# Optimization experiments

Measured on AMD Instinct MI355X. Metric: run time of the kernel, lower is better.

## Reference

```python
import jax, jax.numpy as jnp
import numpy as np

N_NODES = 100000


def _gcn_norm(edges, n_nodes):
    # PyG GCNConv: add self-loops, symmetric normalization D^{-1/2}(A+I)D^{-1/2}
    loop = jnp.arange(n_nodes, dtype=edges.dtype)
    src = jnp.concatenate([edges[0], loop])
    dst = jnp.concatenate([edges[1], loop])
    ones = jnp.ones(src.shape[0], dtype=jnp.float32)
    deg = jax.ops.segment_sum(ones, dst, num_segments=n_nodes)  # >=1 thanks to self-loops
    dinv = jax.lax.rsqrt(deg)
    norm = dinv[src] * dinv[dst]  # [E + N]
    return src, dst, norm


def _gcn_conv(x, W, b, src, dst, norm, n_nodes):
    # lin -> gather -> scale -> scatter-add -> +bias (PyG GCNConv order)
    h = x @ W                                   # [N, D_out]
    msg = h[src] * norm[:, None]                # [E+N, D_out]
    agg = jax.ops.segment_sum(msg, dst, num_segments=n_nodes)
    return agg + b


def setup_inputs() -> dict:
    key = jax.random.key(0)
    k_x, k_e, k_w1, k_w2 = jax.random.split(key, 4)
    F_in, D_hid, n_labels, n_edges = 128, 128, 32, 625000
    features = jax.random.normal(k_x, (N_NODES, F_in), dtype=jnp.float32)
    edges = jax.random.randint(k_e, (2, n_edges), 0, N_NODES, dtype=jnp.int64)
    W1 = jax.random.normal(k_w1, (F_in, D_hid), dtype=jnp.float32) / np.sqrt(F_in)
    b1 = jnp.zeros((D_hid,), dtype=jnp.float32)
    W2 = jax.random.normal(k_w2, (D_hid, n_labels), dtype=jnp.float32) / np.sqrt(D_hid)
    b2 = jnp.zeros((n_labels,), dtype=jnp.float32)
    return {"features": features, "edges": edges, "W1": W1, "b1": b1, "W2": W2, "b2": b2}


def reference(features, edges, W1, b1, W2, b2):
    n_nodes = features.shape[0]
    src, dst, norm = _gcn_norm(edges, n_nodes)
    h1 = jax.nn.relu(_gcn_conv(features, W1, b1, src, dst, norm, n_nodes))
    h2 = _gcn_conv(h1, W2, b2, src, dst, norm, n_nodes)
    return jax.nn.log_softmax(h2, axis=1)
```

## Files before the change

### kernel.cpp

```cpp
#include <hip/hip_runtime.h>

#define NN 100000
#define MAXDEG 32

typedef _Float16 f16;
typedef f16 f16x2 __attribute__((ext_vector_type(2)));
typedef f16 f16x8 __attribute__((ext_vector_type(8)));
typedef float f32x4 __attribute__((ext_vector_type(4)));

__device__ __forceinline__ int detect_is64(const void* edges, int E) {
    const long long* p = (const long long*)edges;
    int m = E < 1024 ? E : 1024;
    int bad = 0;
    for (int i = (threadIdx.x & 63); i < m; i += 64) {
        if ((unsigned long long)p[i] >= (unsigned long long)NN) bad = 1;
    }
    return !__any(bad);
}

__device__ __forceinline__ int edge_at(const void* e, long i, int is64) {
    return is64 ? (int)((const long long*)e)[i] : ((const int*)e)[i];
}

__global__ __launch_bounds__(256) void k_prep(const float* __restrict__ W1,
                                              const float* __restrict__ W2,
                                              f16* __restrict__ BT1,
                                              f16* __restrict__ BT2,
                                              int* __restrict__ deg, int n) {
    int t = blockIdx.x * blockDim.x + threadIdx.x;
    int stride = gridDim.x * blockDim.x;
    for (int i = t; i < n; i += stride) deg[i] = 0;
    for (int i = t; i < 128 * 128; i += stride) {
        int nn = i >> 7, kk = i & 127;
        BT1[i] = (f16)W1[kk * 128 + nn];
    }
    for (int i = t; i < 32 * 128; i += stride) {
        int nn = i >> 7, kk = i & 127;
        BT2[i] = (f16)W2[kk * 32 + nn];
    }
}

__global__ __launch_bounds__(256) void k_dg1(const float* __restrict__ X,
                                             const f16* __restrict__ BT,
                                             f16* __restrict__ H, int n,
                                             const void* edges, int E,
                                             int* __restrict__ deg,
                                             int* __restrict__ slot,
                                             int nG, int nD) {
    __shared__ __align__(16) unsigned char Bs[16384];
    const int bid = blockIdx.x;
    const int lo = nG < nD ? nG : nD;
    int gid = -1, fid = -1;
    if (bid < 2 * lo) {
        if ((bid & 1) == 0) gid = bid >> 1; else fid = bid >> 1;
    } else if (nG > nD) {
        gid = bid - lo;
    } else {
        fid = bid - lo;
    }

    if (fid >= 0) {
        int is64 = detect_is64(edges, E);
        long stride = (long)nD * 256;
        for (long e = (long)fid * 256 + threadIdx.x; e < E; e += stride) {
            int d = edge_at(edges, (long)E + e, is64);
            int t = atomicAdd(&deg[d], 1);
            slot[e] = (t < MAXDEG) ? d * MAXDEG + t : -1;
        }
        return;
    }

    const int tid = threadIdx.x;
    const int wave = tid >> 6;
    const int lane = tid & 63;
    const int lrow = lane & 15;
    const int kgrp = lane >> 4;
    const int row0 = gid * 64 + wave * 16;
    int arow = row0 + lrow;
    if (arow >= n) arow = n - 1;

    f16x8 a[4];
#pragma unroll
    for (int ks = 0; ks < 4; ks++) {
        const float* ap = &X[(long)arow * 128 + ks * 32 + kgrp * 8];
        float4 v0 = *(const float4*)ap;
        float4 v1 = *(const float4*)(ap + 4);
        f16x8 tv;
        tv[0] = (f16)v0.x; tv[1] = (f16)v0.y; tv[2] = (f16)v0.z; tv[3] = (f16)v0.w;
        tv[4] = (f16)v1.x; tv[5] = (f16)v1.y; tv[6] = (f16)v1.z; tv[7] = (f16)v1.w;
        a[ks] = tv;
    }

    const int sw = (lrow & 7) << 4;
#pragma unroll
    for (int half = 0; half < 2; half++) {
#pragma unroll
        for (int s = 0; s < 4; s++) {
            int L = (tid + s * 256) * 16;
            int row = L >> 8;
            f16x8 v = *(const f16x8*)((const unsigned char*)BT + half * 16384 + L);
            *(f16x8*)(Bs + (L ^ ((row & 7) << 4))) = v;
        }
        __syncthreads();
#pragma unroll
        for (int ntl = 0; ntl < 4; ntl++) {
            f32x4 acc = {0.f, 0.f, 0.f, 0.f};
            const int bbase = (ntl * 16 + lrow) * 256 + kgrp * 16;
#pragma unroll
            for (int ks = 0; ks < 4; ks++) {
                f16x8 b = *(const f16x8*)(Bs + ((bbase + ks * 64) ^ sw));
                acc = __builtin_amdgcn_mfma_f32_16x16x32_f16(a[ks], b, acc, 0, 0, 0);
            }
            const int col = (half * 4 + ntl) * 16 + lrow;
#pragma unroll
            for (int r = 0; r < 4; r++) {
                int grow = row0 + kgrp * 4 + r;
                if (grow < n) H[(long)grow * 128 + col] = (f16)acc[r];
            }
        }
        __syncthreads();
    }
}

__global__ void k_fill(const void* edges, int E,
                       const int* __restrict__ slot,
                       int* __restrict__ csr) {
    int is64 = detect_is64(edges, E);
    for (long e = blockIdx.x * (long)blockDim.x + threadIdx.x; e < E;
         e += (long)gridDim.x * blockDim.x) {
        int s = edge_at(edges, e, is64);
        int sl = slot[e];
        if (sl >= 0) csr[sl] = s;
    }
}

__global__ __launch_bounds__(256) void k_sg(const f16* __restrict__ H,
                                            const int* __restrict__ deg,
                                            const int* __restrict__ csr,
                                            const float* __restrict__ b1,
                                            const f16* __restrict__ BT2,
                                            f16* __restrict__ H2, int n) {
    __shared__ __align__(16) unsigned char As[16384];
    __shared__ __align__(16) unsigned char Bs[8192];
    const int tid = threadIdx.x;
    {
        int L = tid * 16;
        int row = L >> 8;
        *(f16x8*)(Bs + (L ^ ((row & 7) << 4))) =
            *(const f16x8*)((const unsigned char*)BT2 + L);
        L += 4096; row = L >> 8;
        *(f16x8*)(Bs + (L ^ ((row & 7) << 4))) =
            *(const f16x8*)((const unsigned char*)BT2 + L);
    }

    const int tile0 = blockIdx.x * 64;
    const int lane16 = tid & 15;
    const int ngrp = tid >> 4;
    const f16x8* H8 = (const f16x8*)H;
    const float4 bl = *(const float4*)&b1[lane16 * 8];
    const float4 bh = *(const float4*)&b1[lane16 * 8 + 4];

#pragma unroll
    for (int sub = 0; sub < 4; sub++) {
        const int lrowA = sub * 16 + ngrp;
        int node = tile0 + lrowA;
        int nd = node < n ? node : n - 1;
        int dg = deg[nd];
        float di = rsqrtf((float)(dg + 1));
        float w0 = di * di;
        f16x8 self = H8[(long)nd * 16 + lane16];
        float acc0[8], acc1[8], acc2[8], acc3[8];
#pragma unroll
        for (int j = 0; j < 8; j++) {
            acc0[j] = w0 * (float)self[j];
            acc1[j] = 0.f; acc2[j] = 0.f; acc3[j] = 0.f;
        }
        int s0 = nd * MAXDEG;
        int cnt = dg < MAXDEG ? dg : MAXDEG;
        int s1 = s0 + cnt;
        for (int i = s0; i < s1; i += 4) {
            int i1 = i + 1 < s1 ? i + 1 : s1 - 1;
            int i2 = i + 2 < s1 ? i + 2 : s1 - 1;
            int i3 = i + 3 < s1 ? i + 3 : s1 - 1;
            int sA = csr[i], sB = csr[i1], sC = csr[i2], sD = csr[i3];
            int dA = deg[sA], dB = deg[sB], dC = deg[sC], dD = deg[sD];
            f16x8 vA = H8[(long)sA * 16 + lane16];
            f16x8 vB = H8[(long)sB * 16 + lane16];
            f16x8 vC = H8[(long)sC * 16 + lane16];
            f16x8 vD = H8[(long)sD * 16 + lane16];
            float wA = rsqrtf((float)(dA + 1)) * di;
            float wB = (i + 1 < s1) ? rsqrtf((float)(dB + 1)) * di : 0.f;
            float wC = (i + 2 < s1) ? rsqrtf((float)(dC + 1)) * di : 0.f;
            float wD = (i + 3 < s1) ? rsqrtf((float)(dD + 1)) * di : 0.f;
#pragma unroll
            for (int j = 0; j < 8; j++) {
                acc0[j] += wA * (float)vA[j];
                acc1[j] += wB * (float)vB[j];
                acc2[j] += wC * (float)vC[j];
                acc3[j] += wD * (float)vD[j];
            }
        }
        f16x8 o;
        o[0] = (f16)fmaxf(acc0[0] + acc1[0] + acc2[0] + acc3[0] + bl.x, 0.f);
        o[1] = (f16)fmaxf(acc0[1] + acc1[1] + acc2[1] + acc3[1] + bl.y, 0.f);
        o[2] = (f16)fmaxf(acc0[2] + acc1[2] + acc2[2] + acc3[2] + bl.z, 0.f);
        o[3] = (f16)fmaxf(acc0[3] + acc1[3] + acc2[3] + acc3[3] + bl.w, 0.f);
        o[4] = (f16)fmaxf(acc0[4] + acc1[4] + acc2[4] + acc3[4] + bh.x, 0.f);
        o[5] = (f16)fmaxf(acc0[5] + acc1[5] + acc2[5] + acc3[5] + bh.y, 0.f);
        o[6] = (f16)fmaxf(acc0[6] + acc1[6] + acc2[6] + acc3[6] + bh.z, 0.f);
        o[7] = (f16)fmaxf(acc0[7] + acc1[7] + acc2[7] + acc3[7] + bh.w, 0.f);
        int L = lrowA * 256 + lane16 * 16;
        *(f16x8*)(As + (L ^ ((lrowA & 7) << 4))) = o;
    }
    __syncthreads();

    const int wave = tid >> 6;
    const int lane = tid & 63;
    const int lrow = lane & 15;
    const int kgrp = lane >> 4;
    const int arowL = wave * 16 + lrow;
    const int swz = (lrow & 7) << 4;

    f16x8 a[4];
#pragma unroll
    for (int ks = 0; ks < 4; ks++)
        a[ks] = *(const f16x8*)(As + ((arowL * 256 + ks * 64 + kgrp * 16) ^ swz));

#pragma unroll
    for (int nt = 0; nt < 2; nt++) {
        f32x4 acc = {0.f, 0.f, 0.f, 0.f};
        const int bbase = (nt * 16 + lrow) * 256 + kgrp * 16;
#pragma unroll
        for (int ks = 0; ks < 4; ks++) {
            f16x8 b = *(const f16x8*)(Bs + ((bbase + ks * 64) ^ swz));
            acc = __builtin_amdgcn_mfma_f32_16x16x32_f16(a[ks], b, acc, 0, 0, 0);
        }
        const int col = nt * 16 + lrow;
#pragma unroll
        for (int r = 0; r < 4; r++) {
            int grow = tile0 + wave * 16 + kgrp * 4 + r;
            if (grow < n) H2[(long)grow * 32 + col] = (f16)acc[r];
        }
    }
}

__global__ __launch_bounds__(256) void k_spmm2(const f16* __restrict__ H,
                                               const int* __restrict__ deg,
                                               const int* __restrict__ csr,
                                               const float* __restrict__ b2,
                                               float* __restrict__ out, int n) {
    const int lane = threadIdx.x & 15;
    const int stot = (gridDim.x * blockDim.x) >> 4;
    const f16x2* H2 = (const f16x2*)H;
    const float2 bias = *(const float2*)&b2[lane * 2];
    for (int node = (blockIdx.x * blockDim.x + threadIdx.x) >> 4; node < n;
         node += stot) {
        int dg = deg[node];
        float di = rsqrtf((float)(dg + 1));
        float w0 = di * di;
        f16x2 self = H2[(long)node * 16 + lane];
        float a0 = w0 * (float)self[0], a1 = w0 * (float)self[1];
        float b0 = 0.f, b1v = 0.f, c0 = 0.f, c1 = 0.f, d0 = 0.f, d1 = 0.f;
        int s0 = node * MAXDEG;
        int cnt = dg < MAXDEG ? dg : MAXDEG;
        int s1 = s0 + cnt;
        for (int i = s0; i < s1; i += 4) {
            int i1 = i + 1 < s1 ? i + 1 : s1 - 1;
            int i2 = i + 2 < s1 ? i + 2 : s1 - 1;
            int i3 = i + 3 < s1 ? i + 3 : s1 - 1;
            int sA = csr[i], sB = csr[i1], sC = csr[i2], sD = csr[i3];
            int dA = deg[sA], dB = deg[sB], dC = deg[sC], dD = deg[sD];
            f16x2 vA = H2[(long)sA * 16 + lane];
            f16x2 vB = H2[(long)sB * 16 + lane];
            f16x2 vC = H2[(long)sC * 16 + lane];
            f16x2 vD = H2[(long)sD * 16 + lane];
            float wA = rsqrtf((float)(dA + 1)) * di;
            float wB = (i + 1 < s1) ? rsqrtf((float)(dB + 1)) * di : 0.f;
            float wC = (i + 2 < s1) ? rsqrtf((float)(dC + 1)) * di : 0.f;
            float wD = (i + 3 < s1) ? rsqrtf((float)(dD + 1)) * di : 0.f;
            a0 += wA * (float)vA[0]; a1 += wA * (float)vA[1];
            b0 += wB * (float)vB[0]; b1v += wB * (float)vB[1];
            c0 += wC * (float)vC[0]; c1 += wC * (float)vC[1];
            d0 += wD * (float)vD[0]; d1 += wD * (float)vD[1];
        }
        float acc0 = a0 + b0 + c0 + d0 + bias.x;
        float acc1 = a1 + b1v + c1 + d1 + bias.y;
        float m = fmaxf(acc0, acc1);
#pragma unroll
        for (int off = 8; off >= 1; off >>= 1) m = fmaxf(m, __shfl_xor(m, off));
        float l = expf(acc0 - m) + expf(acc1 - m);
#pragma unroll
        for (int off = 8; off >= 1; off >>= 1) l += __shfl_xor(l, off);
        float lg = m + logf(l);
        *(float2*)&out[(long)node * 32 + lane * 2] =
            make_float2(acc0 - lg, acc1 - lg);
    }
}

extern "C" void kernel_launch(void* const* d_in, const int* in_sizes, int n_in,
                              void* d_out, int out_size, void* d_ws, size_t ws_size,
                              hipStream_t stream) {
    const float* X  = (const float*)d_in[0];
    const void* edges = d_in[1];
    const float* W1 = (const float*)d_in[2];
    const float* b1 = (const float*)d_in[3];
    const float* W2 = (const float*)d_in[4];
    const float* b2 = (const float*)d_in[5];
    float* out = (float*)d_out;

    const int n = in_sizes[0] / 128;
    const int E = in_sizes[1] / 2;

    char* w = (char*)d_ws;
    auto alloc = [&](size_t bytes) -> char* {
        char* p = w;
        w += (bytes + 511) & ~(size_t)511;
        return p;
    };
    int* deg  = (int*)alloc((size_t)n * 4);
    int* slot = (int*)alloc((size_t)E * 4);
    int* csr  = (int*)alloc((size_t)n * MAXDEG * 4);
    f16* BT1  = (f16*)alloc(128 * 128 * 2);
    f16* BT2  = (f16*)alloc(32 * 128 * 2);
    f16* h1   = (f16*)alloc((size_t)n * 128 * 2);
    f16* h2   = (f16*)alloc((size_t)n * 32 * 2);

    k_prep<<<512, 256, 0, stream>>>(W1, W2, BT1, BT2, deg, n);

    const int nG = (n + 63) / 64;
    const int nD = 2048;
    k_dg1<<<nG + nD, 256, 0, stream>>>(X, BT1, h1, n, edges, E, deg, slot, nG, nD);

    k_fill<<<2048, 256, 0, stream>>>(edges, E, slot, csr);
    k_sg<<<nG, 256, 0, stream>>>(h1, deg, csr, b1, BT2, h2, n);
    k_spmm2<<<2048, 256, 0, stream>>>(h2, deg, csr, b2, out, n);
}
```

Baseline: 112.6 us.

## Split fused degree-count/GEMM kernel into separate degree and GEMM launches

Measured after the change: 127.0 us. 1.13x slower.

```diff
diff --git a/kernel.cpp b/kernel.cpp
--- a/kernel.cpp
+++ b/kernel.cpp
@@ -40,85 +40,14 @@
     }
 }
 
-__global__ __launch_bounds__(256) void k_dg1(const float* __restrict__ X,
-                                             const f16* __restrict__ BT,
-                                             f16* __restrict__ H, int n,
-                                             const void* edges, int E,
-                                             int* __restrict__ deg,
-                                             int* __restrict__ slot,
-                                             int nG, int nD) {
-    __shared__ __align__(16) unsigned char Bs[16384];
-    const int bid = blockIdx.x;
-    const int lo = nG < nD ? nG : nD;
-    int gid = -1, fid = -1;
-    if (bid < 2 * lo) {
-        if ((bid & 1) == 0) gid = bid >> 1; else fid = bid >> 1;
-    } else if (nG > nD) {
-        gid = bid - lo;
-    } else {
-        fid = bid - lo;
-    }
-
-    if (fid >= 0) {
-        int is64 = detect_is64(edges, E);
-        long stride = (long)nD * 256;
-        for (long e = (long)fid * 256 + threadIdx.x; e < E; e += stride) {
-            int d = edge_at(edges, (long)E + e, is64);
-            int t = atomicAdd(&deg[d], 1);
-            slot[e] = (t < MAXDEG) ? d * MAXDEG + t : -1;
-        }
-        return;
-    }
-
-    const int tid = threadIdx.x;
-    const int wave = tid >> 6;
-    const int lane = tid & 63;
-    const int lrow = lane & 15;
-    const int kgrp = lane >> 4;
-    const int row0 = gid * 64 + wave * 16;
-    int arow = row0 + lrow;
-    if (arow >= n) arow = n - 1;
-
-    f16x8 a[4];
-#pragma unroll
-    for (int ks = 0; ks < 4; ks++) {
-        const float* ap = &X[(long)arow * 128 + ks * 32 + kgrp * 8];
-        float4 v0 = *(const float4*)ap;
-        float4 v1 = *(const float4*)(ap + 4);
-        f16x8 tv;
-        tv[0] = (f16)v0.x; tv[1] = (f16)v0.y; tv[2] = (f16)v0.z; tv[3] = (f16)v0.w;
-        tv[4] = (f16)v1.x; tv[5] = (f16)v1.y; tv[6] = (f16)v1.z; tv[7] = (f16)v1.w;
-        a[ks] = tv;
-    }
-
-    const int sw = (lrow & 7) << 4;
-#pragma unroll
-    for (int half = 0; half < 2; half++) {
-#pragma unroll
-        for (int s = 0; s < 4; s++) {
-            int L = (tid + s * 256) * 16;
-            int row = L >> 8;
-            f16x8 v = *(const f16x8*)((const unsigned char*)BT + half * 16384 + L);
-            *(f16x8*)(Bs + (L ^ ((row & 7) << 4))) = v;
-        }
-        __syncthreads();
-#pragma unroll
-        for (int ntl = 0; ntl < 4; ntl++) {
-            f32x4 acc = {0.f, 0.f, 0.f, 0.f};
-            const int bbase = (ntl * 16 + lrow) * 256 + kgrp * 16;
-#pragma unroll
-            for (int ks = 0; ks < 4; ks++) {
-                f16x8 b = *(const f16x8*)(Bs + ((bbase + ks * 64) ^ sw));
-                acc = __builtin_amdgcn_mfma_f32_16x16x32_f16(a[ks], b, acc, 0, 0, 0);
-            }
-            const int col = (half * 4 + ntl) * 16 + lrow;
-#pragma unroll
-            for (int r = 0; r < 4; r++) {
-                int grow = row0 + kgrp * 4 + r;
-                if (grow < n) H[(long)grow * 128 + col] = (f16)acc[r];
-            }
-        }
-        __syncthreads();
+__global__ void k_deg(const void* edges, int E, int* __restrict__ deg,
+                      int* __restrict__ slot) {
+    int is64 = detect_is64(edges, E);
+    for (long e = blockIdx.x * (long)blockDim.x + threadIdx.x; e < E;
+         e += (long)gridDim.x * blockDim.x) {
+        int d = edge_at(edges, (long)E + e, is64);
+        int t = atomicAdd(&deg[d], 1);
+        slot[e] = (t < MAXDEG) ? d * MAXDEG + t : -1;
     }
 }
 
@@ -131,6 +60,62 @@
         int s = edge_at(edges, e, is64);
         int sl = slot[e];
         if (sl >= 0) csr[sl] = s;
+    }
+}
+
+__global__ __launch_bounds__(256) void k_gemm1(const float* __restrict__ X,
+                                               const f16* __restrict__ BT,
+                                               f16* __restrict__ H, int n) {
+    __shared__ __align__(16) unsigned char Bs[16384];
+    const int tid = threadIdx.x;
+    const int wave = tid >> 6;
+    const int lane = tid & 63;
+    const int lrow = lane & 15;
+    const int kgrp = lane >> 4;
+    const int row0 = blockIdx.x * 64 + wave * 16;
+    int arow = row0 + lrow;
+    if (arow >= n) arow = n - 1;
+
+    f16x8 a[4];
+#pragma unroll
+    for (int ks = 0; ks < 4; ks++) {
+        const float* ap = &X[(long)arow * 128 + ks * 32 + kgrp * 8];
+        float4 v0 = *(const float4*)ap;
+        float4 v1 = *(const float4*)(ap + 4);
+        f16x8 tv;
+        tv[0] = (f16)v0.x; tv[1] = (f16)v0.y; tv[2] = (f16)v0.z; tv[3] = (f16)v0.w;
+        tv[4] = (f16)v1.x; tv[5] = (f16)v1.y; tv[6] = (f16)v1.z; tv[7] = (f16)v1.w;
+        a[ks] = tv;
+    }
+
+    const int sw = (lrow & 7) << 4;
+#pragma unroll
+    for (int half = 0; half < 2; half++) {
+#pragma unroll
+        for (int s = 0; s < 4; s++) {
+            int L = (tid + s * 256) * 16;
+            int row = L >> 8;
+            f16x8 v = *(const f16x8*)((const unsigned char*)BT + half * 16384 + L);
+            *(f16x8*)(Bs + (L ^ ((row & 7) << 4))) = v;
+        }
+        __syncthreads();
+#pragma unroll
+        for (int ntl = 0; ntl < 4; ntl++) {
+            f32x4 acc = {0.f, 0.f, 0.f, 0.f};
+            const int bbase = (ntl * 16 + lrow) * 256 + kgrp * 16;
+#pragma unroll
+            for (int ks = 0; ks < 4; ks++) {
+                f16x8 b = *(const f16x8*)(Bs + ((bbase + ks * 64) ^ sw));
+                acc = __builtin_amdgcn_mfma_f32_16x16x32_f16(a[ks], b, acc, 0, 0, 0);
+            }
+            const int col = (half * 4 + ntl) * 16 + lrow;
+#pragma unroll
+            for (int r = 0; r < 4; r++) {
+                int grow = row0 + kgrp * 4 + r;
+                if (grow < n) H[(long)grow * 128 + col] = (f16)acc[r];
+            }
+        }
+        __syncthreads();
     }
 }
 
@@ -326,12 +311,11 @@
     f16* h2   = (f16*)alloc((size_t)n * 32 * 2);
 
     k_prep<<<512, 256, 0, stream>>>(W1, W2, BT1, BT2, deg, n);
+    k_deg<<<2048, 256, 0, stream>>>(edges, E, deg, slot);
+    k_fill<<<2048, 256, 0, stream>>>(edges, E, slot, csr);
 
     const int nG = (n + 63) / 64;
-    const int nD = 2048;
-    k_dg1<<<nG + nD, 256, 0, stream>>>(X, BT1, h1, n, edges, E, deg, slot, nG, nD);
-
-    k_fill<<<2048, 256, 0, stream>>>(edges, E, slot, csr);
+    k_gemm1<<<nG, 256, 0, stream>>>(X, BT1, h1, n);
     k_sg<<<nG, 256, 0, stream>>>(h1, deg, csr, b1, BT2, h2, n);
     k_spmm2<<<2048, 256, 0, stream>>>(h2, deg, csr, b2, out, n);
 }
```
